# Kernel optimization log

Measured on AMD Instinct MI355X. Metric: run time of the kernel, lower is better.

Reference implementation:

```python
import jax, jax.numpy as jnp
import numpy as np

N_USER = 8192
N_PRODUCT = 8192
E = 128
D = 64
K = 32
M = 4


def _make_nbrs(m, n, k, n_other, salt):
    # distinct neighbor indices per (metapath, node): step = n_other // k guarantees
    # the k offsets are distinct modulo n_other (matches set-like ragged lists)
    i = np.arange(m)[:, None, None]
    j = np.arange(n)[None, :, None]
    t = np.arange(k)[None, None, :]
    idx = (j * 7 + i * 131 + salt * 17 + t * (n_other // k)) % n_other
    return jnp.asarray(idx, dtype=jnp.int32)


def setup_inputs() -> dict:
    key = jax.random.key(0)
    ks = jax.random.split(key, 16)
    s = 0.1
    return {
        "user": jax.random.normal(ks[0], (N_USER, E), jnp.float32),
        "product": jax.random.normal(ks[1], (N_PRODUCT, E), jnp.float32),
        "V": jax.random.normal(ks[2], (2, M, E, D), jnp.float32) * s,
        "X": jax.random.normal(ks[3], (2, M, 1, D), jnp.float32) * s,
        "W_p": jax.random.normal(ks[4], (2, M, E, D), jnp.float32) * s,
        "B_p": jax.random.normal(ks[5], (2, M, D), jnp.float32) * s,
        "W_q": jax.random.normal(ks[6], (2, M, E, D), jnp.float32) * s,
        "B_q": jax.random.normal(ks[7], (2, M, D), jnp.float32) * s,
        "Q": jax.random.normal(ks[8], (2, M, 1, D), jnp.float32) * s,
        "user_nbrs": _make_nbrs(M, N_USER, K, N_PRODUCT, 0),
        "product_nbrs": _make_nbrs(M, N_PRODUCT, K, N_USER, 1),
    }


def _phase(src, other, nbrs, v, x, w, b, wq, bq, q):
    # src: [n,E], other: [n_other,E], nbrs: [M,n,K] indices into other
    m, n, k = nbrs.shape
    n_other = other.shape[0]
    nbr_emb = other[nbrs]  # [M,n,K,E] ragged gather
    proj_src = jnp.einsum('ne,med->mnd', src, v)          # [M,n,D]
    proj_nbr = jnp.einsum('mnke,med->mnkd', nbr_emb, w)   # [M,n,K,D]
    h = jnp.tanh(proj_src[:, :, None, :] + proj_nbr + b[:, None, None, :])
    scores = jnp.einsum('mnkd,md->mnk', h, x[:, 0])       # [M,n,K]
    # Faithful to torch: non-neighbor logit is -1e-9 for metapath 0; for
    # metapath i>=1 the repeated whole-tensor softmax makes it 1/n_other.
    baseline = jnp.where(jnp.arange(m) == 0,
                         jnp.float32(-1e-9),
                         jnp.float32(1.0) / n_other)      # [M]
    mx = jnp.maximum(scores.max(-1), baseline[:, None])   # [M,n]
    e = jnp.exp(scores - mx[..., None])
    denom = e.sum(-1) + (n_other - k) * jnp.exp(baseline[:, None] - mx)
    A = e / denom[..., None]                              # softmax over full axis
    # H aggregation uses detached attention weights (A.data in torch)
    H = src[None] + jnp.einsum('mnk,mnke->mne', jax.lax.stop_gradient(A), nbr_emb)
    sem = jnp.tanh(jnp.einsum('mne,med->mnd', H, wq) + bq[:, None, :])
    beta_raw = jax.lax.stop_gradient(
        jnp.einsum('mnd,md->mn', sem, q[:, 0]).mean(-1))  # [M], detached (.data)
    beta = jax.nn.softmax(beta_raw)
    return jnp.einsum('m,mne->ne', beta, H)


def reference(user, product, V, X, W_p, B_p, W_q, B_q, Q, user_nbrs, product_nbrs):
    user_out = _phase(user, product, user_nbrs,
                      V[0], X[0], W_p[0], B_p[0], W_q[0], B_q[0], Q[0])
    # product phase attends over the UPDATED user embeddings
    product_out = _phase(product, user_out, product_nbrs,
                         V[1], X[1], W_p[1], B_p[1], W_q[1], B_q[1], Q[1])
    return (user_out, product_out)
```

## Files before the change

### kernel.cpp

```cpp
#include <hip/hip_runtime.h>
#include <hip/hip_bf16.h>

#define NN 8192
#define ED 128
#define DD 64
#define KK 32
#define MM 4

typedef __attribute__((ext_vector_type(8))) short short8;
typedef __attribute__((ext_vector_type(4))) float f32x4;

#if __has_builtin(__builtin_amdgcn_exp2f)
#define EXP2R(x) __builtin_amdgcn_exp2f(x)
#else
#define EXP2R(x) __expf((x) * 0.6931471805599453f)
#endif
#define C2LOG2E 2.8853900817779268f

__device__ __forceinline__ float ftanh_pre(float v)
{
    return fmaf(-2.0f, __builtin_amdgcn_rcpf(EXP2R(v) + 1.0f), 1.0f);
}
__device__ __forceinline__ float ftanh(float x)
{
    return ftanh_pre(x * C2LOG2E);
}

__device__ __forceinline__ unsigned short f2bf(float x)
{
    __hip_bfloat16 b = __float2bfloat16(x);
    return *reinterpret_cast<unsigned short*>(&b);
}
__device__ __forceinline__ float bflo(unsigned int u) { return __uint_as_float(u << 16); }
__device__ __forceinline__ float bfhi(unsigned int u) { return __uint_as_float(u & 0xFFFF0000u); }
__device__ __forceinline__ float readlane_f(float v, int lane)
{
    return __uint_as_float(__builtin_amdgcn_readlane(__float_as_uint(v), lane));
}

__global__ __launch_bounds__(256) void prep_kernel(
    const float* __restrict__ user, unsigned short* __restrict__ userB,
    const float* __restrict__ product, unsigned short* __restrict__ productB,
    const float* __restrict__ V, unsigned short* __restrict__ VT,
    const float* __restrict__ Wp, unsigned short* __restrict__ PT,
    const float* __restrict__ Wq, unsigned short* __restrict__ QT)
{
    const int y = blockIdx.y;
    if (y < 2) {
        const float* in = y ? product : user;
        unsigned short* out = y ? productB : userB;
        const int i = blockIdx.x * 256 + threadIdx.x;
        const float4 v = ((const float4*)in)[i];
        uint2 o;
        o.x = (unsigned int)f2bf(v.x) | ((unsigned int)f2bf(v.y) << 16);
        o.y = (unsigned int)f2bf(v.z) | ((unsigned int)f2bf(v.w) << 16);
        ((uint2*)out)[i] = o;
    } else {
        if (blockIdx.x >= 256) return;
        const float* in = (y == 2) ? V : (y == 3) ? Wp : Wq;
        unsigned short* out = (y == 2) ? VT : (y == 3) ? PT : QT;
        const int gid = blockIdx.x * 256 + threadIdx.x;
        const int s   = gid >> 13;
        const int rem = gid & 8191;
        const int e   = rem >> 6;
        const int d   = rem & 63;
        out[((size_t)s * DD + d) * ED + e] = f2bf(in[gid]);
    }
}

__global__ __launch_bounds__(256) void proj2_mfma(
    const unsigned short* __restrict__ emb0,
    const unsigned short* __restrict__ Wt0,
    const float* __restrict__ Bias0,
    float* __restrict__ outF0,
    const unsigned short* __restrict__ emb1,
    const unsigned short* __restrict__ Wt1,
    unsigned short* __restrict__ outB1)
{
    const int z    = blockIdx.z;
    const int m    = blockIdx.y;
    const int tid  = threadIdx.x;
    const int wave = tid >> 6;
    const int lane = tid & 63;
    const int nrow = lane & 15;
    const int quad = lane >> 4;
    const int r0   = blockIdx.x * 64 + wave * 16;

    const unsigned short* embB = z ? emb1 : emb0;
    const unsigned short* WtB  = z ? Wt1 : Wt0;

    const short8* A8 = (const short8*)(embB + (size_t)(r0 + nrow) * ED);
    const short8* B8 = (const short8*)(WtB + (size_t)m * DD * ED);

    f32x4 acc0 = {0.f, 0.f, 0.f, 0.f};
    f32x4 acc1 = {0.f, 0.f, 0.f, 0.f};
    f32x4 acc2 = {0.f, 0.f, 0.f, 0.f};
    f32x4 acc3 = {0.f, 0.f, 0.f, 0.f};

    #pragma unroll
    for (int kq = 0; kq < 4; ++kq) {
        const short8 a = A8[kq * 4 + quad];
        const short8 b0 = B8[(0 * 16 + nrow) * 16 + kq * 4 + quad];
        const short8 b1 = B8[(1 * 16 + nrow) * 16 + kq * 4 + quad];
        const short8 b2 = B8[(2 * 16 + nrow) * 16 + kq * 4 + quad];
        const short8 b3 = B8[(3 * 16 + nrow) * 16 + kq * 4 + quad];
        acc0 = __builtin_amdgcn_mfma_f32_16x16x32_bf16(a, b0, acc0, 0, 0, 0);
        acc1 = __builtin_amdgcn_mfma_f32_16x16x32_bf16(a, b1, acc1, 0, 0, 0);
        acc2 = __builtin_amdgcn_mfma_f32_16x16x32_bf16(a, b2, acc2, 0, 0, 0);
        acc3 = __builtin_amdgcn_mfma_f32_16x16x32_bf16(a, b3, acc3, 0, 0, 0);
    }

    f32x4 accs[4] = {acc0, acc1, acc2, acc3};
    if (z == 0) {
        #pragma unroll
        for (int t = 0; t < 4; ++t) {
            const int d = t * 16 + nrow;
            const float bv = Bias0[m * DD + d];
            #pragma unroll
            for (int reg = 0; reg < 4; ++reg) {
                const int r = r0 + quad * 4 + reg;
                outF0[((size_t)m * NN + r) * DD + d] =
                    (accs[t][reg] + bv) * C2LOG2E;
            }
        }
    } else {
        #pragma unroll
        for (int t = 0; t < 4; ++t) {
            const int d = t * 16 + nrow;
            #pragma unroll
            for (int reg = 0; reg < 4; ++reg) {
                const int r = r0 + quad * 4 + reg;
                outB1[((size_t)m * NN + r) * DD + d] = f2bf(accs[t][reg]);
            }
        }
    }
}

__global__ __launch_bounds__(256) void attn_kernel(
    const float* __restrict__ src,
    const unsigned short* __restrict__ otherB,
    const int*   __restrict__ nbrs,
    const float* __restrict__ S,
    const unsigned short* __restrict__ PnB,
    const float* __restrict__ Xv,
    unsigned short* __restrict__ HoutB)
{
    const int m    = blockIdx.y;
    const int tid  = threadIdx.x;
    const int w    = tid >> 6;
    const int lane = tid & 63;
    const int g    = blockIdx.x * 4 + w;
    const int j0   = g * 2;
    const int j1   = g * 2 + 1;

    const int kr = lane >> 3;
    const int d8 = lane & 7;

    const int jj = (lane < 32) ? j0 : j1;
    const int idxreg = nbrs[((size_t)m * NN + jj) * KK + (lane & 31)];

    float S0c[8], S1c[8], m2X[8];
    float sumX;
    {
        const float4 a0 = *(const float4*)(S + ((size_t)m * NN + j0) * DD + d8 * 8);
        const float4 a1 = *(const float4*)(S + ((size_t)m * NN + j0) * DD + d8 * 8 + 4);
        const float4 b0 = *(const float4*)(S + ((size_t)m * NN + j1) * DD + d8 * 8);
        const float4 b1 = *(const float4*)(S + ((size_t)m * NN + j1) * DD + d8 * 8 + 4);
        const float4 x0 = *(const float4*)(Xv + (size_t)m * DD + d8 * 8);
        const float4 x1 = *(const float4*)(Xv + (size_t)m * DD + d8 * 8 + 4);
        S0c[0]=a0.x; S0c[1]=a0.y; S0c[2]=a0.z; S0c[3]=a0.w;
        S0c[4]=a1.x; S0c[5]=a1.y; S0c[6]=a1.z; S0c[7]=a1.w;
        S1c[0]=b0.x; S1c[1]=b0.y; S1c[2]=b0.z; S1c[3]=b0.w;
        S1c[4]=b1.x; S1c[5]=b1.y; S1c[6]=b1.z; S1c[7]=b1.w;
        m2X[0]=-2.0f*x0.x; m2X[1]=-2.0f*x0.y; m2X[2]=-2.0f*x0.z; m2X[3]=-2.0f*x0.w;
        m2X[4]=-2.0f*x1.x; m2X[5]=-2.0f*x1.y; m2X[6]=-2.0f*x1.z; m2X[7]=-2.0f*x1.w;
        sumX = ((x0.x + x0.y) + (x0.z + x0.w)) + ((x1.x + x1.y) + (x1.z + x1.w));
    }
    const float2 hs0 = ((const float2*)(src + (size_t)j0 * ED))[lane];
    const float2 hs1 = ((const float2*)(src + (size_t)j1 * ED))[lane];

    float ea0[4], ea1[4];
    #pragma unroll
    for (int i = 0; i < 4; ++i) {
        const int k   = i * 8 + kr;
        const int jk0 = __shfl(idxreg, k, 64);
        const int jk1 = __shfl(idxreg, 32 + k, 64);
        const uint4 p0 = ((const uint4*)(PnB + ((size_t)m * NN + jk0) * DD))[d8];
        const uint4 p1 = ((const uint4*)(PnB + ((size_t)m * NN + jk1) * DD))[d8];
        const unsigned int pw0[4] = {p0.x, p0.y, p0.z, p0.w};
        const unsigned int pw1[4] = {p1.x, p1.y, p1.z, p1.w};
        float q0 = sumX, q1 = sumX;
        #pragma unroll
        for (int c = 0; c < 4; ++c) {
            const float lo0 = bflo(pw0[c]), hi0 = bfhi(pw0[c]);
            const float lo1 = bflo(pw1[c]), hi1 = bfhi(pw1[c]);
            float r;
            r = __builtin_amdgcn_rcpf(EXP2R(fmaf(lo0, C2LOG2E, S0c[c*2  ])) + 1.0f);
            q0 = fmaf(m2X[c*2  ], r, q0);
            r = __builtin_amdgcn_rcpf(EXP2R(fmaf(lo1, C2LOG2E, S1c[c*2  ])) + 1.0f);
            q1 = fmaf(m2X[c*2  ], r, q1);
            r = __builtin_amdgcn_rcpf(EXP2R(fmaf(hi0, C2LOG2E, S0c[c*2+1])) + 1.0f);
            q0 = fmaf(m2X[c*2+1], r, q0);
            r = __builtin_amdgcn_rcpf(EXP2R(fmaf(hi1, C2LOG2E, S1c[c*2+1])) + 1.0f);
            q1 = fmaf(m2X[c*2+1], r, q1);
        }
        q0 += __shfl_xor(q0, 1, 64);  q1 += __shfl_xor(q1, 1, 64);
        q0 += __shfl_xor(q0, 2, 64);  q1 += __shfl_xor(q1, 2, 64);
        q0 += __shfl_xor(q0, 4, 64);  q1 += __shfl_xor(q1, 4, 64);
        ea0[i] = q0;
        ea1[i] = q1;
    }

    const float baseline = (m == 0) ? -1e-9f : (1.0f / (float)NN);
    float mx0 = ea0[0], mx1 = ea1[0];
    #pragma unroll
    for (int i = 1; i < 4; ++i) { mx0 = fmaxf(mx0, ea0[i]); mx1 = fmaxf(mx1, ea1[i]); }
    mx0 = fmaxf(mx0, __shfl_xor(mx0, 8, 64));
    mx1 = fmaxf(mx1, __shfl_xor(mx1, 8, 64));
    mx0 = fmaxf(mx0, __shfl_xor(mx0, 16, 64));
    mx1 = fmaxf(mx1, __shfl_xor(mx1, 16, 64));
    mx0 = fmaxf(mx0, __shfl_xor(mx0, 32, 64));
    mx1 = fmaxf(mx1, __shfl_xor(mx1, 32, 64));
    mx0 = fmaxf(mx0, baseline);
    mx1 = fmaxf(mx1, baseline);
    float sum0 = 0.0f, sum1 = 0.0f;
    #pragma unroll
    for (int i = 0; i < 4; ++i) {
        ea0[i] = __expf(ea0[i] - mx0); sum0 += ea0[i];
        ea1[i] = __expf(ea1[i] - mx1); sum1 += ea1[i];
    }
    sum0 += __shfl_xor(sum0, 8, 64);   sum1 += __shfl_xor(sum1, 8, 64);
    sum0 += __shfl_xor(sum0, 16, 64);  sum1 += __shfl_xor(sum1, 16, 64);
    sum0 += __shfl_xor(sum0, 32, 64);  sum1 += __shfl_xor(sum1, 32, 64);
    const float inv0 =
        __builtin_amdgcn_rcpf(sum0 + (float)(NN - KK) * __expf(baseline - mx0));
    const float inv1 =
        __builtin_amdgcn_rcpf(sum1 + (float)(NN - KK) * __expf(baseline - mx1));
    #pragma unroll
    for (int i = 0; i < 4; ++i) { ea0[i] *= inv0; ea1[i] *= inv1; }

    float2 ha = hs0, hb = hs1;
    #pragma unroll
    for (int k = 0; k < KK; ++k) {
        const float a0 = readlane_f(ea0[k >> 3], (k & 7) * 8);
        const float a1 = readlane_f(ea1[k >> 3], (k & 7) * 8);
        const int  jk0 = __builtin_amdgcn_readlane(idxreg, k);
        const int  jk1 = __builtin_amdgcn_readlane(idxreg, 32 + k);
        const unsigned int o0 = ((const unsigned int*)(otherB + (size_t)jk0 * ED))[lane];
        const unsigned int o1 = ((const unsigned int*)(otherB + (size_t)jk1 * ED))[lane];
        ha.x = fmaf(a0, bflo(o0), ha.x);
        hb.x = fmaf(a1, bflo(o1), hb.x);
        ha.y = fmaf(a0, bfhi(o0), ha.y);
        hb.y = fmaf(a1, bfhi(o1), hb.y);
    }
    const unsigned int hu0 =
        (unsigned int)f2bf(ha.x) | ((unsigned int)f2bf(ha.y) << 16);
    const unsigned int hu1 =
        (unsigned int)f2bf(hb.x) | ((unsigned int)f2bf(hb.y) << 16);
    ((unsigned int*)(HoutB + ((size_t)m * NN + j0) * ED))[lane] = hu0;
    ((unsigned int*)(HoutB + ((size_t)m * NN + j1) * ED))[lane] = hu1;
}

__global__ __launch_bounds__(256) void sem_mfma(
    const unsigned short* __restrict__ HB,
    const unsigned short* __restrict__ WqT,
    const float* __restrict__ Bq,
    const float* __restrict__ Qv,
    float* __restrict__ bp)
{
    const int m    = blockIdx.y;
    const int tid  = threadIdx.x;
    const int wave = tid >> 6;
    const int lane = tid & 63;
    const int nrow = lane & 15;
    const int quad = lane >> 4;
    const int r0   = blockIdx.x * 64 + wave * 16;

    __shared__ float red_sh[4];

    const short8* A8 = (const short8*)(HB + ((size_t)m * NN + r0 + nrow) * ED);
    const short8* B8 = (const short8*)(WqT + (size_t)m * DD * ED);

    f32x4 acc0 = {0.f, 0.f, 0.f, 0.f};
    f32x4 acc1 = {0.f, 0.f, 0.f, 0.f};
    f32x4 acc2 = {0.f, 0.f, 0.f, 0.f};
    f32x4 acc3 = {0.f, 0.f, 0.f, 0.f};

    #pragma unroll
    for (int kq = 0; kq < 4; ++kq) {
        const short8 a = A8[kq * 4 + quad];
        const short8 b0 = B8[(0 * 16 + nrow) * 16 + kq * 4 + quad];
        const short8 b1 = B8[(1 * 16 + nrow) * 16 + kq * 4 + quad];
        const short8 b2 = B8[(2 * 16 + nrow) * 16 + kq * 4 + quad];
        const short8 b3 = B8[(3 * 16 + nrow) * 16 + kq * 4 + quad];
        acc0 = __builtin_amdgcn_mfma_f32_16x16x32_bf16(a, b0, acc0, 0, 0, 0);
        acc1 = __builtin_amdgcn_mfma_f32_16x16x32_bf16(a, b1, acc1, 0, 0, 0);
        acc2 = __builtin_amdgcn_mfma_f32_16x16x32_bf16(a, b2, acc2, 0, 0, 0);
        acc3 = __builtin_amdgcn_mfma_f32_16x16x32_bf16(a, b3, acc3, 0, 0, 0);
    }

    f32x4 accs[4] = {acc0, acc1, acc2, acc3};
    float part = 0.0f;
    #pragma unroll
    for (int t = 0; t < 4; ++t) {
        const int d = t * 16 + nrow;
        const float bq = Bq[m * DD + d];
        const float qv = Qv[m * DD + d];
        #pragma unroll
        for (int reg = 0; reg < 4; ++reg)
            part = fmaf(ftanh(accs[t][reg] + bq), qv, part);
    }
    #pragma unroll
    for (int off = 32; off; off >>= 1) part += __shfl_xor(part, off, 64);
    if (lane == 0) red_sh[wave] = part;
    __syncthreads();
    if (tid == 0)
        bp[m * 128 + blockIdx.x] =
            (red_sh[0] + red_sh[1]) + (red_sh[2] + red_sh[3]);
}

__global__ __launch_bounds__(256) void combine_kernel(
    const unsigned short* __restrict__ HB,
    const float* __restrict__ bp,
    float* __restrict__ outp,
    unsigned short* __restrict__ outB)
{
    __shared__ float bw_sh[4];
    const int tid = threadIdx.x;
    if (tid < 64) {
        const int m = tid >> 4, t = tid & 15;
        float s = 0.0f;
        #pragma unroll
        for (int i = 0; i < 8; ++i)
            s += bp[m * 128 + t + i * 16];
        s += __shfl_xor(s, 1, 64);
        s += __shfl_xor(s, 2, 64);
        s += __shfl_xor(s, 4, 64);
        s += __shfl_xor(s, 8, 64);
        const float v = s * (1.0f / (float)NN);
        float mx = v;
        mx = fmaxf(mx, __shfl_xor(mx, 16, 64));
        mx = fmaxf(mx, __shfl_xor(mx, 32, 64));
        const float e = expf(v - mx);
        float es = e;
        es += __shfl_xor(es, 16, 64);
        es += __shfl_xor(es, 32, 64);
        if (t == 0) bw_sh[m] = e / es;
    }
    __syncthreads();

    const int i = blockIdx.x * 256 + tid;
    const size_t st = (size_t)NN * ED / 4;
    const uint2* h = (const uint2*)HB;
    float r0 = 0.f, r1 = 0.f, r2 = 0.f, r3 = 0.f;
    #pragma unroll
    for (int s = 0; s < MM; ++s) {
        const float b = bw_sh[s];
        const uint2 v = h[s * st + i];
        r0 = fmaf(b, bflo(v.x), r0);
        r1 = fmaf(b, bfhi(v.x), r1);
        r2 = fmaf(b, bflo(v.y), r2);
        r3 = fmaf(b, bfhi(v.y), r3);
    }
    float4 o; o.x = r0; o.y = r1; o.z = r2; o.w = r3;
    ((float4*)outp)[i] = o;
    if (outB) {
        uint2 ob;
        ob.x = (unsigned int)f2bf(r0) | ((unsigned int)f2bf(r1) << 16);
        ob.y = (unsigned int)f2bf(r2) | ((unsigned int)f2bf(r3) << 16);
        ((uint2*)outB)[i] = ob;
    }
}

extern "C" void kernel_launch(void* const* d_in, const int* in_sizes, int n_in,
                              void* d_out, int out_size, void* d_ws, size_t ws_size,
                              hipStream_t stream)
{
    const float* user    = (const float*)d_in[0];
    const float* product = (const float*)d_in[1];
    const float* V   = (const float*)d_in[2];
    const float* X   = (const float*)d_in[3];
    const float* W_p = (const float*)d_in[4];
    const float* B_p = (const float*)d_in[5];
    const float* W_q = (const float*)d_in[6];
    const float* B_q = (const float*)d_in[7];
    const float* Q   = (const float*)d_in[8];
    const int* user_nbrs    = (const int*)d_in[9];
    const int* product_nbrs = (const int*)d_in[10];

    float* out  = (float*)d_out;
    float* out0 = out;
    float* out1 = out + (size_t)NN * ED;

    float* ws = (float*)d_ws;
    float* bp = ws;
    float* S  = bp + 1024;
    unsigned short* us = (unsigned short*)(S + (size_t)MM * NN * DD);
    unsigned short* PnB      = us;
    unsigned short* HB       = PnB + (size_t)MM * NN * DD;
    unsigned short* userB    = HB + (size_t)MM * NN * ED;
    unsigned short* productB = userB + (size_t)NN * ED;
    unsigned short* oB       = productB + (size_t)NN * ED;
    unsigned short* VT       = oB + (size_t)NN * ED;
    unsigned short* PT       = VT + (size_t)2 * MM * DD * ED;
    unsigned short* QT       = PT + (size_t)2 * MM * DD * ED;

    const size_t MED = (size_t)MM * ED * DD;
    const size_t MD  = (size_t)MM * DD;

    const dim3 gM2(NN / 64, MM, 2);
    const dim3 gM(NN / 64, MM);
    const dim3 gA(NN / 8, MM);
    const int cBlocks = (NN * ED / 4) / 256;

    prep_kernel<<<dim3(1024, 5), 256, 0, stream>>>(user, userB, product, productB,
                                                   V, VT, W_p, PT, W_q, QT);

    {
        proj2_mfma<<<gM2, 256, 0, stream>>>(userB, VT, B_p, S,
                                            productB, PT, PnB);
        attn_kernel<<<gA, 256, 0, stream>>>(user, productB, user_nbrs,
                                            S, PnB, X, HB);
        sem_mfma<<<gM, 256, 0, stream>>>(HB, QT, B_q, Q, bp);
        combine_kernel<<<cBlocks, 256, 0, stream>>>(HB, bp, out0, oB);
    }

    {
        proj2_mfma<<<gM2, 256, 0, stream>>>(productB, VT + MED, B_p + MD, S,
                                            oB, PT + MED, PnB);
        attn_kernel<<<gA, 256, 0, stream>>>(product, oB, product_nbrs,
                                            S, PnB, X + MD, HB);
        sem_mfma<<<gM, 256, 0, stream>>>(HB, QT + MED, B_q + MD, Q + MD, bp);
        combine_kernel<<<cBlocks, 256, 0, stream>>>(HB, bp, out1, nullptr);
    }
}
```

Before: 203.6 us.

## Fuse semantic-attention MFMA into attention kernel via shared-memory H tile

Merges sem_mfma into the attention kernel. Blocks grow to 512 threads covering 16 nodes, and each block stages its H rows in LDS. Four waves then run the 16x64 bf16 MFMA, apply tanh and the q-dot, and write one partial sum per block. This removes one kernel launch per phase and the global re-read of H for the semantic projection, at the cost of a block-wide barrier, idle waves during the MFMA step, and a larger partial-sum buffer for combine to reduce.

Result: faster. 195.9 us (-3.8%).

```diff
diff --git a/kernel.cpp b/kernel.cpp
--- a/kernel.cpp
+++ b/kernel.cpp
@@ -136,20 +136,27 @@
     }
 }
 
-__global__ __launch_bounds__(256) void attn_kernel(
+__global__ __launch_bounds__(512) void attn_sem_kernel(
     const float* __restrict__ src,
     const unsigned short* __restrict__ otherB,
     const int*   __restrict__ nbrs,
     const float* __restrict__ S,
     const unsigned short* __restrict__ PnB,
     const float* __restrict__ Xv,
-    unsigned short* __restrict__ HoutB)
-{
+    unsigned short* __restrict__ HoutB,
+    const unsigned short* __restrict__ WqT,
+    const float* __restrict__ Bq,
+    const float* __restrict__ Qv,
+    float* __restrict__ bp)
+{
+    __shared__ __align__(16) unsigned int lh[16][68];
+    __shared__ float red_sh[4];
+
     const int m    = blockIdx.y;
     const int tid  = threadIdx.x;
     const int w    = tid >> 6;
     const int lane = tid & 63;
-    const int g    = blockIdx.x * 4 + w;
+    const int g    = blockIdx.x * 8 + w;
     const int j0   = g * 2;
     const int j1   = g * 2 + 1;
 
@@ -259,63 +266,37 @@
         (unsigned int)f2bf(hb.x) | ((unsigned int)f2bf(hb.y) << 16);
     ((unsigned int*)(HoutB + ((size_t)m * NN + j0) * ED))[lane] = hu0;
     ((unsigned int*)(HoutB + ((size_t)m * NN + j1) * ED))[lane] = hu1;
-}
-
-__global__ __launch_bounds__(256) void sem_mfma(
-    const unsigned short* __restrict__ HB,
-    const unsigned short* __restrict__ WqT,
-    const float* __restrict__ Bq,
-    const float* __restrict__ Qv,
-    float* __restrict__ bp)
-{
-    const int m    = blockIdx.y;
-    const int tid  = threadIdx.x;
-    const int wave = tid >> 6;
-    const int lane = tid & 63;
-    const int nrow = lane & 15;
-    const int quad = lane >> 4;
-    const int r0   = blockIdx.x * 64 + wave * 16;
-
-    __shared__ float red_sh[4];
-
-    const short8* A8 = (const short8*)(HB + ((size_t)m * NN + r0 + nrow) * ED);
-    const short8* B8 = (const short8*)(WqT + (size_t)m * DD * ED);
-
-    f32x4 acc0 = {0.f, 0.f, 0.f, 0.f};
-    f32x4 acc1 = {0.f, 0.f, 0.f, 0.f};
-    f32x4 acc2 = {0.f, 0.f, 0.f, 0.f};
-    f32x4 acc3 = {0.f, 0.f, 0.f, 0.f};
-
-    #pragma unroll
-    for (int kq = 0; kq < 4; ++kq) {
-        const short8 a = A8[kq * 4 + quad];
-        const short8 b0 = B8[(0 * 16 + nrow) * 16 + kq * 4 + quad];
-        const short8 b1 = B8[(1 * 16 + nrow) * 16 + kq * 4 + quad];
-        const short8 b2 = B8[(2 * 16 + nrow) * 16 + kq * 4 + quad];
-        const short8 b3 = B8[(3 * 16 + nrow) * 16 + kq * 4 + quad];
-        acc0 = __builtin_amdgcn_mfma_f32_16x16x32_bf16(a, b0, acc0, 0, 0, 0);
-        acc1 = __builtin_amdgcn_mfma_f32_16x16x32_bf16(a, b1, acc1, 0, 0, 0);
-        acc2 = __builtin_amdgcn_mfma_f32_16x16x32_bf16(a, b2, acc2, 0, 0, 0);
-        acc3 = __builtin_amdgcn_mfma_f32_16x16x32_bf16(a, b3, acc3, 0, 0, 0);
-    }
-
-    f32x4 accs[4] = {acc0, acc1, acc2, acc3};
-    float part = 0.0f;
-    #pragma unroll
-    for (int t = 0; t < 4; ++t) {
-        const int d = t * 16 + nrow;
+
+    lh[w * 2    ][lane] = hu0;
+    lh[w * 2 + 1][lane] = hu1;
+    __syncthreads();
+
+    if (w < 4) {
+        const int nrow = lane & 15;
+        const int quad = lane >> 4;
+        const short8* B8 = (const short8*)(WqT + (size_t)m * DD * ED);
+        const short8* A8 = (const short8*)&lh[nrow][0];
+        f32x4 acc = {0.f, 0.f, 0.f, 0.f};
+        #pragma unroll
+        for (int kq = 0; kq < 4; ++kq) {
+            const short8 a = A8[kq * 4 + quad];
+            const short8 b = B8[(w * 16 + nrow) * 16 + kq * 4 + quad];
+            acc = __builtin_amdgcn_mfma_f32_16x16x32_bf16(a, b, acc, 0, 0, 0);
+        }
+        const int d = w * 16 + nrow;
         const float bq = Bq[m * DD + d];
         const float qv = Qv[m * DD + d];
+        float part = 0.0f;
         #pragma unroll
         for (int reg = 0; reg < 4; ++reg)
-            part = fmaf(ftanh(accs[t][reg] + bq), qv, part);
-    }
-    #pragma unroll
-    for (int off = 32; off; off >>= 1) part += __shfl_xor(part, off, 64);
-    if (lane == 0) red_sh[wave] = part;
+            part = fmaf(ftanh(acc[reg] + bq), qv, part);
+        #pragma unroll
+        for (int off = 32; off; off >>= 1) part += __shfl_xor(part, off, 64);
+        if (lane == 0) red_sh[w] = part;
+    }
     __syncthreads();
     if (tid == 0)
-        bp[m * 128 + blockIdx.x] =
+        bp[m * 512 + blockIdx.x] =
             (red_sh[0] + red_sh[1]) + (red_sh[2] + red_sh[3]);
 }
 
@@ -331,8 +312,8 @@
         const int m = tid >> 4, t = tid & 15;
         float s = 0.0f;
         #pragma unroll
-        for (int i = 0; i < 8; ++i)
-            s += bp[m * 128 + t + i * 16];
+        for (int i = 0; i < 32; ++i)
+            s += bp[m * 512 + t + i * 16];
         s += __shfl_xor(s, 1, 64);
         s += __shfl_xor(s, 2, 64);
         s += __shfl_xor(s, 4, 64);
@@ -394,7 +375,7 @@
 
     float* ws = (float*)d_ws;
     float* bp = ws;
-    float* S  = bp + 1024;
+    float* S  = bp + 2048;
     unsigned short* us = (unsigned short*)(S + (size_t)MM * NN * DD);
     unsigned short* PnB      = us;
     unsigned short* HB       = PnB + (size_t)MM * NN * DD;
@@ -409,8 +390,7 @@
     const size_t MD  = (size_t)MM * DD;
 
     const dim3 gM2(NN / 64, MM, 2);
-    const dim3 gM(NN / 64, MM);
-    const dim3 gA(NN / 8, MM);
+    const dim3 gA(NN / 16, MM);
     const int cBlocks = (NN * ED / 4) / 256;
 
     prep_kernel<<<dim3(1024, 5), 256, 0, stream>>>(user, userB, product, productB,
@@ -419,18 +399,18 @@
     {
         proj2_mfma<<<gM2, 256, 0, stream>>>(userB, VT, B_p, S,
                                             productB, PT, PnB);
-        attn_kernel<<<gA, 256, 0, stream>>>(user, productB, user_nbrs,
-                                            S, PnB, X, HB);
-        sem_mfma<<<gM, 256, 0, stream>>>(HB, QT, B_q, Q, bp);
+        attn_sem_kernel<<<gA, 512, 0, stream>>>(user, productB, user_nbrs,
+                                                S, PnB, X, HB,
+                                                QT, B_q, Q, bp);
         combine_kernel<<<cBlocks, 256, 0, stream>>>(HB, bp, out0, oB);
     }
 
     {
         proj2_mfma<<<gM2, 256, 0, stream>>>(productB, VT + MED, B_p + MD, S,
                                             oB, PT + MED, PnB);
-        attn_kernel<<<gA, 256, 0, stream>>>(product, oB, product_nbrs,
-                                            S, PnB, X + MD, HB);
-        sem_mfma<<<gM, 256, 0, stream>>>(HB, QT + MED, B_q + MD, Q + MD, bp);
+        attn_sem_kernel<<<gA, 512, 0, stream>>>(product, oB, product_nbrs,
+                                                S, PnB, X + MD, HB,
+                                                QT + MED, B_q + MD, Q + MD, bp);
         combine_kernel<<<cBlocks, 256, 0, stream>>>(HB, bp, out1, nullptr);
     }
 }
```
